# Kernel tuning notes

Measured on AMD Instinct MI355X. Metric: run time of the kernel, lower is better.

Reference implementation:

```python
import jax, jax.numpy as jnp
import numpy as np

N_NODES = 50000


def gcn_conv(x, W, b, edge_index, n_nodes):
    """torch_geometric GCNConv: linear -> symmetric-normalized scatter-add with self-loops."""
    h = x @ W  # [N, out]
    src = jnp.concatenate([edge_index[0], jnp.arange(n_nodes)])  # add self-loops
    dst = jnp.concatenate([edge_index[1], jnp.arange(n_nodes)])
    deg = jax.ops.segment_sum(jnp.ones_like(dst, dtype=h.dtype), dst, num_segments=n_nodes)
    dinv = jnp.where(deg > 0, jax.lax.rsqrt(deg), 0.0)  # deg^-1/2, inf -> 0
    norm = dinv[src] * dinv[dst]                         # [E+N]
    msg = h[src] * norm[:, None]                         # gather + scale
    out = jax.ops.segment_sum(msg, dst, num_segments=n_nodes)  # scatter-add
    return out + b


def setup_inputs() -> dict:
    key = jax.random.key(0)
    k1, k2, k3, k4, k5, k6 = jax.random.split(key, 6)
    nhid, nfeat = 128, 256
    E = 800000
    x = jax.random.normal(k1, (N_NODES, nhid), dtype=jnp.float32)
    edge_index = jax.random.randint(k2, (2, E), 0, N_NODES, dtype=jnp.int64)
    s1 = 1.0 / np.sqrt(nhid)
    W1 = jax.random.uniform(k3, (nhid, nhid), jnp.float32, -s1, s1)
    b1 = jnp.zeros((nhid,), jnp.float32)
    W2 = jax.random.uniform(k4, (nhid, nfeat), jnp.float32, -s1, s1)
    b2 = jnp.zeros((nfeat,), jnp.float32)
    return {"x": x, "edge_index": edge_index, "W1": W1, "b1": b1, "W2": W2, "b2": b2}


def reference(x, edge_index, W1, b1, W2, b2):
    # eval mode: dropout is identity
    h = jax.nn.relu(gcn_conv(x, W1, b1, edge_index, N_NODES))
    out = jax.nn.relu(gcn_conv(h, W2, b2, edge_index, N_NODES))
    return out
```

## Files before the change

kernel.cpp:

```cpp
#include <hip/hip_runtime.h>


typedef __attribute__((ext_vector_type(8))) _Float16 half8;
typedef __attribute__((ext_vector_type(4))) _Float16 half4v;
typedef __attribute__((ext_vector_type(4))) float floatx4;

#define BSHIFT 7
#define BNODES 128

__global__ __launch_bounds__(256) void count_conv_kernel(const int* __restrict__ dst,
                                                         int* __restrict__ bucket_cnt,
                                                         const float* __restrict__ W1,
                                                         const float* __restrict__ W2,
                                                         _Float16* __restrict__ wt1,
                                                         _Float16* __restrict__ wt2,
                                                         int E, int chunk, int NB) {
    int t = threadIdx.x;
    if (blockIdx.x >= 256) {
        int idx = (blockIdx.x - 256) * 256 + t;
        if (idx < 128 * 128) {
            int nn = idx >> 7, k = idx & 127;
            wt1[idx] = (_Float16)W1[k * 128 + nn];
        } else if (idx < (128 + 256) * 128) {
            int j = idx - 128 * 128;
            int nn = j >> 7, k = j & 127;
            wt2[j] = (_Float16)W2[k * 256 + nn];
        }
        return;
    }
    extern __shared__ int hist[];
    for (int i = t; i < NB; i += 256) hist[i] = 0;
    __syncthreads();
    int cbeg = blockIdx.x * chunk;
    int cend = min(E, cbeg + chunk);
    for (int e = cbeg + t; e < cend; e += 256)
        atomicAdd(&hist[dst[e] >> BSHIFT], 1);
    __syncthreads();
    for (int i = t; i < NB; i += 256)
        if (hist[i]) atomicAdd(&bucket_cnt[i], hist[i]);
}

__global__ void bucket_scan_kernel(const int* __restrict__ bucket_cnt,
                                   int* __restrict__ bucket_base,
                                   int* __restrict__ bucket_cursor, int NB) {
    __shared__ int sd[512];
    int t = threadIdx.x;
    int v = (t < NB) ? bucket_cnt[t] : 0;
    sd[t] = v;
    __syncthreads();
    for (int off = 1; off < 512; off <<= 1) {
        int x = (t >= off) ? sd[t - off] : 0;
        __syncthreads();
        sd[t] += x;
        __syncthreads();
    }
    if (t < NB) {
        int excl = sd[t] - v;
        bucket_base[t] = excl;
        bucket_cursor[t] = excl;
        if (t == NB - 1) bucket_base[NB] = sd[t];
    }
}

__global__ __launch_bounds__(256) void bucket_scatter_kernel(const int* __restrict__ src,
                                                             const int* __restrict__ dst,
                                                             int* __restrict__ bucket_cursor,
                                                             unsigned* __restrict__ bucketed,
                                                             int E, int chunk, int NB) {
    extern __shared__ int sh[];
    int* hist = sh;
    int* base_loc = sh + NB;
    int* cur2 = sh + 2 * NB;
    int t = threadIdx.x;
    for (int i = t; i < NB; i += 256) { hist[i] = 0; cur2[i] = 0; }
    __syncthreads();
    int cbeg = blockIdx.x * chunk;
    int cend = min(E, cbeg + chunk);
    for (int e = cbeg + t; e < cend; e += 256)
        atomicAdd(&hist[dst[e] >> BSHIFT], 1);
    __syncthreads();
    for (int i = t; i < NB; i += 256) {
        int c = hist[i];
        base_loc[i] = c ? atomicAdd(&bucket_cursor[i], c) : 0;
    }
    __syncthreads();
    for (int e = cbeg + t; e < cend; e += 256) {
        int d = dst[e];
        int bkt = d >> BSHIFT;
        int r = atomicAdd(&cur2[bkt], 1);
        bucketed[base_loc[bkt] + r] =
            (unsigned)src[e] | ((unsigned)(d & (BNODES - 1)) << 16);
    }
}

__global__ __launch_bounds__(256) void build_kernel(const unsigned* __restrict__ bucketed,
                                                    const int* __restrict__ bucket_base,
                                                    const float* __restrict__ x,
                                                    int* __restrict__ rowstart,
                                                    float* __restrict__ dinv,
                                                    int* __restrict__ csr,
                                                    _Float16* __restrict__ xs,
                                                    int N, int E, int NB) {
    __shared__ int deg_loc[BNODES];
    __shared__ int tmp[BNODES];
    __shared__ int cur_loc[BNODES];
    __shared__ float dinv_loc[BNODES];
    int t = threadIdx.x;
    int b = blockIdx.x;
    int n0 = b << BSHIFT;
    int nodes_in = min(BNODES, N - n0);
    int wbeg = bucket_base[b];
    int wend = bucket_base[b + 1];

    if (t < BNODES) deg_loc[t] = 0;
    __syncthreads();
    for (int e = wbeg + t; e < wend; e += 256)
        atomicAdd(&deg_loc[bucketed[e] >> 16], 1);
    __syncthreads();
    if (t < BNODES) tmp[t] = deg_loc[t];
    __syncthreads();
    for (int off = 1; off < BNODES; off <<= 1) {
        int v = 0;
        if (t < BNODES && t >= off) v = tmp[t - off];
        __syncthreads();
        if (t < BNODES) tmp[t] += v;
        __syncthreads();
    }
    if (t < BNODES) {
        int abs0 = wbeg + tmp[t] - deg_loc[t];
        cur_loc[t] = abs0;
        float dv = rsqrtf((float)(deg_loc[t] + 1));
        dinv_loc[t] = dv;
        if (t < nodes_in) {
            rowstart[n0 + t] = abs0;
            dinv[n0 + t] = dv;
        }
    }
    if (b == NB - 1 && t == 0) rowstart[N] = E;
    __syncthreads();
    for (int e = wbeg + t; e < wend; e += 256) {
        unsigned u2 = bucketed[e];
        int pos = atomicAdd(&cur_loc[u2 >> 16], 1);
        csr[pos] = (int)(u2 & 0xFFFFu);
    }
    int total4 = nodes_in * 32;
    const float4* x4 = (const float4*)(x + (size_t)n0 * 128);
    for (int i = t; i < total4; i += 256) {
        int row = i >> 5;
        float dv = dinv_loc[row];
        float4 v = x4[i];
        half4v h;
        h[0] = (_Float16)(v.x * dv); h[1] = (_Float16)(v.y * dv);
        h[2] = (_Float16)(v.z * dv); h[3] = (_Float16)(v.w * dv);
        *(half4v*)(xs + (size_t)n0 * 128 + (size_t)i * 4) = h;
    }
}

__global__ __launch_bounds__(256) void agg128_kernel(const _Float16* __restrict__ g,
                                                     const int* __restrict__ rowstart,
                                                     const int* __restrict__ csr,
                                                     const float* __restrict__ dinv,
                                                     _Float16* __restrict__ out, int n) {
    int wid = (blockIdx.x * blockDim.x + threadIdx.x) >> 6;
    int lane = threadIdx.x & 63;
    if (wid >= n) return;
    int q = lane >> 4, l16 = lane & 15;
    int beg = rowstart[wid], end = rowstart[wid + 1];

    float a[8] = {0.f, 0.f, 0.f, 0.f, 0.f, 0.f, 0.f, 0.f};
    if (q == 0) {
        half8 v = *(const half8*)(g + (size_t)wid * 128 + l16 * 8);
#pragma unroll
        for (int j = 0; j < 8; j++) a[j] = (float)v[j];
    }
    int e = beg + q;
    for (; e + 12 < end; e += 16) {
        int u0 = csr[e];
        int u1 = csr[e + 4];
        int u2 = csr[e + 8];
        int u3 = csr[e + 12];
        half8 v0 = *(const half8*)(g + (size_t)u0 * 128 + l16 * 8);
        half8 v1 = *(const half8*)(g + (size_t)u1 * 128 + l16 * 8);
        half8 v2 = *(const half8*)(g + (size_t)u2 * 128 + l16 * 8);
        half8 v3 = *(const half8*)(g + (size_t)u3 * 128 + l16 * 8);
#pragma unroll
        for (int j = 0; j < 8; j++)
            a[j] += ((float)v0[j] + (float)v1[j]) + ((float)v2[j] + (float)v3[j]);
    }
    for (; e + 4 < end; e += 8) {
        int u0 = csr[e];
        int u1 = csr[e + 4];
        half8 v0 = *(const half8*)(g + (size_t)u0 * 128 + l16 * 8);
        half8 v1 = *(const half8*)(g + (size_t)u1 * 128 + l16 * 8);
#pragma unroll
        for (int j = 0; j < 8; j++) a[j] += (float)v0[j] + (float)v1[j];
    }
    for (; e < end; e += 4) {
        int u = csr[e];
        half8 v = *(const half8*)(g + (size_t)u * 128 + l16 * 8);
#pragma unroll
        for (int j = 0; j < 8; j++) a[j] += (float)v[j];
    }
#pragma unroll
    for (int j = 0; j < 8; j++) {
        a[j] += __shfl_xor(a[j], 16);
        a[j] += __shfl_xor(a[j], 32);
    }
    if (q == 0) {
        float dv = dinv[wid];
        half8 o;
#pragma unroll
        for (int j = 0; j < 8; j++) o[j] = (_Float16)(a[j] * dv);
        *(half8*)(out + (size_t)wid * 128 + l16 * 8) = o;
    }
}

template <bool HALF_OUT>
__global__ __launch_bounds__(256) void gemm_kernel(const _Float16* __restrict__ A,
                                                   const _Float16* __restrict__ Bt,
                                                   const float* __restrict__ bias,
                                                   const float* __restrict__ dinv,
                                                   void* __restrict__ outp,
                                                   int n, int nout) {
    __shared__ _Float16 As[128][136];
    __shared__ _Float16 Bs[128][136];
    int t = threadIdx.x;
    int row0 = blockIdx.x * 128;
    int col0 = blockIdx.y * 128;

#pragma unroll
    for (int i = 0; i < 8; i++) {
        int c = i * 256 + t;
        int r = c >> 4, seg = c & 15;
        int gr = row0 + r;
        if (gr >= n) gr = n - 1;
        uint4 v = *(const uint4*)(A + (size_t)gr * 128 + seg * 8);
        *(uint4*)(&As[r][seg * 8]) = v;
    }
#pragma unroll
    for (int i = 0; i < 8; i++) {
        int c = i * 256 + t;
        int r = c >> 4, seg = c & 15;
        uint4 v = *(const uint4*)(Bt + (size_t)(col0 + r) * 128 + seg * 8);
        *(uint4*)(&Bs[r][seg * 8]) = v;
    }
    __syncthreads();

    int wid = t >> 6, lane = t & 63;
    int wm = wid >> 1, wn = wid & 1;
    int quad = lane >> 4, l16 = lane & 15;

    floatx4 acc[4][4];
#pragma unroll
    for (int mt = 0; mt < 4; mt++)
#pragma unroll
        for (int nt = 0; nt < 4; nt++) acc[mt][nt] = (floatx4){0.f, 0.f, 0.f, 0.f};

#pragma unroll
    for (int ks = 0; ks < 4; ks++) {
        int k0 = ks * 32 + quad * 8;
        half8 a[4], b[4];
#pragma unroll
        for (int mt = 0; mt < 4; mt++)
            a[mt] = *(const half8*)(&As[wm * 64 + mt * 16 + l16][k0]);
#pragma unroll
        for (int nt = 0; nt < 4; nt++)
            b[nt] = *(const half8*)(&Bs[wn * 64 + nt * 16 + l16][k0]);
#pragma unroll
        for (int mt = 0; mt < 4; mt++)
#pragma unroll
            for (int nt = 0; nt < 4; nt++)
                acc[mt][nt] = __builtin_amdgcn_mfma_f32_16x16x32_f16(a[mt], b[nt], acc[mt][nt], 0, 0, 0);
    }

#pragma unroll
    for (int mt = 0; mt < 4; mt++) {
        int rbase = row0 + wm * 64 + mt * 16 + quad * 4;
#pragma unroll
        for (int reg = 0; reg < 4; reg++) {
            int r = rbase + reg;
            if (r < n) {
                float dv = HALF_OUT ? dinv[r] : 1.f;
#pragma unroll
                for (int nt = 0; nt < 4; nt++) {
                    int cc = col0 + wn * 64 + nt * 16 + l16;
                    float val = fmaxf(acc[mt][nt][reg] + bias[cc], 0.f);
                    if (HALF_OUT)
                        ((_Float16*)outp)[(size_t)r * nout + cc] = (_Float16)(val * dv);
                    else
                        ((float*)outp)[(size_t)r * nout + cc] = val;
                }
            }
        }
    }
}

extern "C" void kernel_launch(void* const* d_in, const int* in_sizes, int n_in,
                              void* d_out, int out_size, void* d_ws, size_t ws_size,
                              hipStream_t stream) {
    const float* x  = (const float*)d_in[0];
    const int*   ei = (const int*)d_in[1];
    const float* W1 = (const float*)d_in[2];
    const float* b1 = (const float*)d_in[3];
    const float* W2 = (const float*)d_in[4];
    const float* b2 = (const float*)d_in[5];
    float* out = (float*)d_out;

    int N = in_sizes[0] / 128;
    int E = in_sizes[1] / 2;
    const int* src = ei;
    const int* dst = ei + E;
    int NB = (N + BNODES - 1) >> BSHIFT;

    char* w = (char*)d_ws;
    size_t off = 0;
    auto alloc = [&](size_t bytes) -> char* {
        char* p = w + off;
        off = (off + bytes + 255) & ~(size_t)255;
        return p;
    };
    int*      bucket_cnt    = (int*)alloc((size_t)NB * 4);
    int*      bucket_base   = (int*)alloc((size_t)(NB + 1) * 4);
    int*      bucket_cursor = (int*)alloc((size_t)NB * 4);
    unsigned* bucketed      = (unsigned*)alloc((size_t)E * 4);
    int*      rowstart      = (int*)alloc((size_t)(N + 1) * 4);
    float*    dinv          = (float*)alloc((size_t)N * 4);
    int*      csr           = (int*)alloc((size_t)E * 4);
    _Float16* wt1           = (_Float16*)alloc((size_t)128 * 128 * 2);
    _Float16* wt2           = (_Float16*)alloc((size_t)256 * 128 * 2);
    _Float16* xs            = (_Float16*)alloc((size_t)N * 128 * 2);
    _Float16* q1            = (_Float16*)alloc((size_t)N * 128 * 2);
    _Float16* p2            = (_Float16*)alloc((size_t)N * 128 * 2);
    _Float16* q2            = (_Float16*)alloc((size_t)N * 128 * 2);

    int chunk = (E + 255) / 256;
    size_t lds1 = (size_t)NB * 4;
    size_t lds3 = (size_t)NB * 12;

    hipMemsetAsync(bucket_cnt, 0, (size_t)NB * 4, stream);
    hipLaunchKernelGGL(count_conv_kernel, dim3(256 + 192), dim3(256), lds1, stream,
                       dst, bucket_cnt, W1, W2, wt1, wt2, E, chunk, NB);
    hipLaunchKernelGGL(bucket_scan_kernel, dim3(1), dim3(512), 0, stream, bucket_cnt, bucket_base, bucket_cursor, NB);
    hipLaunchKernelGGL(bucket_scatter_kernel, dim3(256), dim3(256), lds3, stream, src, dst, bucket_cursor, bucketed, E, chunk, NB);
    hipLaunchKernelGGL(build_kernel, dim3(NB), dim3(256), 0, stream, bucketed, bucket_base, x, rowstart, dinv, csr, xs, N, E, NB);

    int gbm = (N + 127) / 128;
    int nb_agg = (N + 3) / 4;
    hipLaunchKernelGGL(agg128_kernel, dim3(nb_agg), dim3(256), 0, stream, xs, rowstart, csr, dinv, q1, N);
    hipLaunchKernelGGL((gemm_kernel<true>), dim3(gbm, 1), dim3(256), 0, stream, q1, wt1, b1, dinv, (void*)p2, N, 128);
    hipLaunchKernelGGL(agg128_kernel, dim3(nb_agg), dim3(256), 0, stream, p2, rowstart, csr, dinv, q2, N);
    hipLaunchKernelGGL((gemm_kernel<false>), dim3(gbm, 2), dim3(256), 0, stream, q2, wt2, b2, dinv, (void*)out, N, 256);
}
```

Measured before the change: 224.8 us.

## Fuse neighbor aggregation into GEMM kernel, aggregating 128-row tile into LDS

Replaces the separate aggregation and GEMM kernels with one fused kernel per layer. Each block aggregates its 128 rows into LDS using half-waves of 32 lanes, then runs MFMA against weights read straight from global memory. For the second layer, one block loops over both 128-column output tiles. This removes the fp16 intermediate write and reread and two kernel launches. In exchange, each block has only 391 blocks' worth of parallelism and processes its rows serially (16 rows per half-wave), which hurts latency hiding for the gather. It also loses the LDS staging of B.

```diff
diff --git a/kernel.cpp b/kernel.cpp
--- a/kernel.cpp
+++ b/kernel.cpp
@@ -156,93 +156,55 @@
     }
 }
 
-__global__ __launch_bounds__(256) void agg128_kernel(const _Float16* __restrict__ g,
-                                                     const int* __restrict__ rowstart,
-                                                     const int* __restrict__ csr,
-                                                     const float* __restrict__ dinv,
-                                                     _Float16* __restrict__ out, int n) {
-    int wid = (blockIdx.x * blockDim.x + threadIdx.x) >> 6;
-    int lane = threadIdx.x & 63;
-    if (wid >= n) return;
-    int q = lane >> 4, l16 = lane & 15;
-    int beg = rowstart[wid], end = rowstart[wid + 1];
-
-    float a[8] = {0.f, 0.f, 0.f, 0.f, 0.f, 0.f, 0.f, 0.f};
-    if (q == 0) {
-        half8 v = *(const half8*)(g + (size_t)wid * 128 + l16 * 8);
-#pragma unroll
-        for (int j = 0; j < 8; j++) a[j] = (float)v[j];
-    }
-    int e = beg + q;
-    for (; e + 12 < end; e += 16) {
-        int u0 = csr[e];
-        int u1 = csr[e + 4];
-        int u2 = csr[e + 8];
-        int u3 = csr[e + 12];
-        half8 v0 = *(const half8*)(g + (size_t)u0 * 128 + l16 * 8);
-        half8 v1 = *(const half8*)(g + (size_t)u1 * 128 + l16 * 8);
-        half8 v2 = *(const half8*)(g + (size_t)u2 * 128 + l16 * 8);
-        half8 v3 = *(const half8*)(g + (size_t)u3 * 128 + l16 * 8);
-#pragma unroll
-        for (int j = 0; j < 8; j++)
-            a[j] += ((float)v0[j] + (float)v1[j]) + ((float)v2[j] + (float)v3[j]);
-    }
-    for (; e + 4 < end; e += 8) {
-        int u0 = csr[e];
-        int u1 = csr[e + 4];
-        half8 v0 = *(const half8*)(g + (size_t)u0 * 128 + l16 * 8);
-        half8 v1 = *(const half8*)(g + (size_t)u1 * 128 + l16 * 8);
-#pragma unroll
-        for (int j = 0; j < 8; j++) a[j] += (float)v0[j] + (float)v1[j];
-    }
-    for (; e < end; e += 4) {
-        int u = csr[e];
-        half8 v = *(const half8*)(g + (size_t)u * 128 + l16 * 8);
-#pragma unroll
-        for (int j = 0; j < 8; j++) a[j] += (float)v[j];
-    }
-#pragma unroll
-    for (int j = 0; j < 8; j++) {
-        a[j] += __shfl_xor(a[j], 16);
-        a[j] += __shfl_xor(a[j], 32);
-    }
-    if (q == 0) {
-        float dv = dinv[wid];
-        half8 o;
-#pragma unroll
-        for (int j = 0; j < 8; j++) o[j] = (_Float16)(a[j] * dv);
-        *(half8*)(out + (size_t)wid * 128 + l16 * 8) = o;
-    }
-}
-
-template <bool HALF_OUT>
-__global__ __launch_bounds__(256) void gemm_kernel(const _Float16* __restrict__ A,
-                                                   const _Float16* __restrict__ Bt,
-                                                   const float* __restrict__ bias,
-                                                   const float* __restrict__ dinv,
-                                                   void* __restrict__ outp,
-                                                   int n, int nout) {
-    __shared__ _Float16 As[128][136];
-    __shared__ _Float16 Bs[128][136];
+template <int NCT, bool HALF_OUT>
+__global__ __launch_bounds__(256) void fused_kernel(const _Float16* __restrict__ g,
+                                                    const int* __restrict__ rowstart,
+                                                    const int* __restrict__ csr,
+                                                    const float* __restrict__ dinv,
+                                                    const _Float16* __restrict__ Bt,
+                                                    const float* __restrict__ bias,
+                                                    void* __restrict__ outp,
+                                                    int n) {
+    __shared__ _Float16 As[128][132];
     int t = threadIdx.x;
     int row0 = blockIdx.x * 128;
-    int col0 = blockIdx.y * 128;
-
-#pragma unroll
-    for (int i = 0; i < 8; i++) {
-        int c = i * 256 + t;
-        int r = c >> 4, seg = c & 15;
-        int gr = row0 + r;
-        if (gr >= n) gr = n - 1;
-        uint4 v = *(const uint4*)(A + (size_t)gr * 128 + seg * 8);
-        *(uint4*)(&As[r][seg * 8]) = v;
-    }
-#pragma unroll
-    for (int i = 0; i < 8; i++) {
-        int c = i * 256 + t;
-        int r = c >> 4, seg = c & 15;
-        uint4 v = *(const uint4*)(Bt + (size_t)(col0 + r) * 128 + seg * 8);
-        *(uint4*)(&Bs[r][seg * 8]) = v;
+    int hw = t >> 5, l32 = t & 31;
+
+#pragma unroll 1
+    for (int r8 = 0; r8 < 16; r8++) {
+        int rl = hw * 16 + r8;
+        int row = row0 + rl;
+        float a0 = 0.f, a1 = 0.f, a2 = 0.f, a3 = 0.f;
+        if (row < n) {
+            int beg = rowstart[row], end = rowstart[row + 1];
+            half4v s = *(const half4v*)(g + (size_t)row * 128 + l32 * 4);
+            a0 = (float)s[0]; a1 = (float)s[1]; a2 = (float)s[2]; a3 = (float)s[3];
+            int e = beg;
+            for (; e + 3 < end; e += 4) {
+                int u0 = csr[e];
+                int u1 = csr[e + 1];
+                int u2 = csr[e + 2];
+                int u3 = csr[e + 3];
+                half4v v0 = *(const half4v*)(g + (size_t)u0 * 128 + l32 * 4);
+                half4v v1 = *(const half4v*)(g + (size_t)u1 * 128 + l32 * 4);
+                half4v v2 = *(const half4v*)(g + (size_t)u2 * 128 + l32 * 4);
+                half4v v3 = *(const half4v*)(g + (size_t)u3 * 128 + l32 * 4);
+                a0 += ((float)v0[0] + (float)v1[0]) + ((float)v2[0] + (float)v3[0]);
+                a1 += ((float)v0[1] + (float)v1[1]) + ((float)v2[1] + (float)v3[1]);
+                a2 += ((float)v0[2] + (float)v1[2]) + ((float)v2[2] + (float)v3[2]);
+                a3 += ((float)v0[3] + (float)v1[3]) + ((float)v2[3] + (float)v3[3]);
+            }
+            for (; e < end; ++e) {
+                int u = csr[e];
+                half4v v = *(const half4v*)(g + (size_t)u * 128 + l32 * 4);
+                a0 += (float)v[0]; a1 += (float)v[1]; a2 += (float)v[2]; a3 += (float)v[3];
+            }
+            float dv = dinv[row];
+            a0 *= dv; a1 *= dv; a2 *= dv; a3 *= dv;
+        }
+        half4v h;
+        h[0] = (_Float16)a0; h[1] = (_Float16)a1; h[2] = (_Float16)a2; h[3] = (_Float16)a3;
+        *(half4v*)(&As[rl][l32 * 4]) = h;
     }
     __syncthreads();
 
@@ -250,45 +212,49 @@
     int wm = wid >> 1, wn = wid & 1;
     int quad = lane >> 4, l16 = lane & 15;
 
-    floatx4 acc[4][4];
-#pragma unroll
-    for (int mt = 0; mt < 4; mt++)
-#pragma unroll
-        for (int nt = 0; nt < 4; nt++) acc[mt][nt] = (floatx4){0.f, 0.f, 0.f, 0.f};
-
-#pragma unroll
-    for (int ks = 0; ks < 4; ks++) {
-        int k0 = ks * 32 + quad * 8;
-        half8 a[4], b[4];
+#pragma unroll 1
+    for (int ct = 0; ct < NCT; ct++) {
+        int col0 = ct * 128;
+        floatx4 acc[4][4];
 #pragma unroll
         for (int mt = 0; mt < 4; mt++)
-            a[mt] = *(const half8*)(&As[wm * 64 + mt * 16 + l16][k0]);
-#pragma unroll
-        for (int nt = 0; nt < 4; nt++)
-            b[nt] = *(const half8*)(&Bs[wn * 64 + nt * 16 + l16][k0]);
-#pragma unroll
-        for (int mt = 0; mt < 4; mt++)
+#pragma unroll
+            for (int nt = 0; nt < 4; nt++) acc[mt][nt] = (floatx4){0.f, 0.f, 0.f, 0.f};
+
+#pragma unroll
+        for (int ks = 0; ks < 4; ks++) {
+            int k0 = ks * 32 + quad * 8;
+            half8 a[4], b[4];
 #pragma unroll
             for (int nt = 0; nt < 4; nt++)
-                acc[mt][nt] = __builtin_amdgcn_mfma_f32_16x16x32_f16(a[mt], b[nt], acc[mt][nt], 0, 0, 0);
-    }
-
-#pragma unroll
-    for (int mt = 0; mt < 4; mt++) {
-        int rbase = row0 + wm * 64 + mt * 16 + quad * 4;
-#pragma unroll
-        for (int reg = 0; reg < 4; reg++) {
-            int r = rbase + reg;
-            if (r < n) {
-                float dv = HALF_OUT ? dinv[r] : 1.f;
-#pragma unroll
-                for (int nt = 0; nt < 4; nt++) {
-                    int cc = col0 + wn * 64 + nt * 16 + l16;
-                    float val = fmaxf(acc[mt][nt][reg] + bias[cc], 0.f);
-                    if (HALF_OUT)
-                        ((_Float16*)outp)[(size_t)r * nout + cc] = (_Float16)(val * dv);
-                    else
-                        ((float*)outp)[(size_t)r * nout + cc] = val;
+                b[nt] = *(const half8*)(Bt + (size_t)(col0 + wn * 64 + nt * 16 + l16) * 128 + k0);
+#pragma unroll
+            for (int mt = 0; mt < 4; mt++)
+                a[mt] = *(const half8*)(&As[wm * 64 + mt * 16 + l16][k0]);
+#pragma unroll
+            for (int mt = 0; mt < 4; mt++)
+#pragma unroll
+                for (int nt = 0; nt < 4; nt++)
+                    acc[mt][nt] = __builtin_amdgcn_mfma_f32_16x16x32_f16(a[mt], b[nt], acc[mt][nt], 0, 0, 0);
+        }
+
+#pragma unroll
+        for (int mt = 0; mt < 4; mt++) {
+            int rbase = row0 + wm * 64 + mt * 16 + quad * 4;
+#pragma unroll
+            for (int reg = 0; reg < 4; reg++) {
+                int r = rbase + reg;
+                if (r < n) {
+                    float dv = HALF_OUT ? dinv[r] : 1.f;
+#pragma unroll
+                    for (int nt = 0; nt < 4; nt++) {
+                        int cc = col0 + wn * 64 + nt * 16 + l16;
+                        float val = fmaxf(acc[mt][nt][reg] + bias[cc], 0.f);
+                        if (HALF_OUT)
+                            ((_Float16*)outp)[(size_t)r * (NCT * 128) + cc] = (_Float16)(val * dv);
+                        else
+                            ((float*)outp)[(size_t)r * (NCT * 128) + cc] = val;
+                    }
                 }
             }
         }
@@ -329,9 +295,7 @@
     _Float16* wt1           = (_Float16*)alloc((size_t)128 * 128 * 2);
     _Float16* wt2           = (_Float16*)alloc((size_t)256 * 128 * 2);
     _Float16* xs            = (_Float16*)alloc((size_t)N * 128 * 2);
-    _Float16* q1            = (_Float16*)alloc((size_t)N * 128 * 2);
     _Float16* p2            = (_Float16*)alloc((size_t)N * 128 * 2);
-    _Float16* q2            = (_Float16*)alloc((size_t)N * 128 * 2);
 
     int chunk = (E + 255) / 256;
     size_t lds1 = (size_t)NB * 4;
@@ -345,9 +309,8 @@
     hipLaunchKernelGGL(build_kernel, dim3(NB), dim3(256), 0, stream, bucketed, bucket_base, x, rowstart, dinv, csr, xs, N, E, NB);
 
     int gbm = (N + 127) / 128;
-    int nb_agg = (N + 3) / 4;
-    hipLaunchKernelGGL(agg128_kernel, dim3(nb_agg), dim3(256), 0, stream, xs, rowstart, csr, dinv, q1, N);
-    hipLaunchKernelGGL((gemm_kernel<true>), dim3(gbm, 1), dim3(256), 0, stream, q1, wt1, b1, dinv, (void*)p2, N, 128);
-    hipLaunchKernelGGL(agg128_kernel, dim3(nb_agg), dim3(256), 0, stream, p2, rowstart, csr, dinv, q2, N);
-    hipLaunchKernelGGL((gemm_kernel<false>), dim3(gbm, 2), dim3(256), 0, stream, q2, wt2, b2, dinv, (void*)out, N, 256);
-}
+    hipLaunchKernelGGL((fused_kernel<1, true>), dim3(gbm), dim3(256), 0, stream,
+                       xs, rowstart, csr, dinv, wt1, b1, (void*)p2, N);
+    hipLaunchKernelGGL((fused_kernel<2, false>), dim3(gbm), dim3(256), 0, stream,
+                       p2, rowstart, csr, dinv, wt2, b2, (void*)out, N);
+}
```

Measured after the change: 328.7 us. 1.46x slower.
